# Performance work log

Hardware: AMD Instinct MI355X
Metric: run time of the kernel (lower is better)

## Reference

```python
import jax, jax.numpy as jnp
import numpy as np

SOM = (32, 32)   # som_dim; SOM[0]*SOM[1] == num_embeddings
LR = 0.05


def setup_inputs() -> dict:
    key = jax.random.key(0)
    k1, k2 = jax.random.split(key)
    B, K, D = 65536, 1024, 256
    x = jax.random.normal(k1, (B, D), dtype=jnp.float32)
    embeddings = jax.random.uniform(k2, (K, D), dtype=jnp.float32)  # torch.rand init
    return {"x": x, "embeddings": embeddings}


def reference(x, embeddings):
    K, D = embeddings.shape
    # pairwise squared distances: [B, K]
    dist = (jnp.sum(x * x, axis=1, keepdims=True)
            + jnp.sum(embeddings * embeddings, axis=1)
            - 2.0 * (x @ embeddings.T))
    n_min = jnp.argmin(dist, axis=1)          # [B]
    z_q = embeddings[n_min]                   # [B, D]

    # SOM grid coordinates and clamped neighbors
    n_x = n_min // SOM[1]
    n_y = n_min % SOM[1]
    x_up = jnp.where(n_x < SOM[0] - 1, n_x + 1, n_x)
    x_down = jnp.where(n_x > 0, n_x - 1, n_x)
    y_right = jnp.where(n_y < SOM[1] - 1, n_y + 1, n_y)
    y_left = jnp.where(n_y > 0, n_y - 1, n_y)
    idx_up = x_up * SOM[1] + n_y
    idx_down = x_down * SOM[1] + n_y
    idx_right = n_x * SOM[1] + y_right
    idx_left = n_x * SOM[1] + y_left

    # [B, 4, D] neighbor gather (order: up, down, left, right as in torch code)
    nbr_idx = jnp.stack([idx_up, idx_down, idx_left, idx_right], axis=1)
    z_q_neighbors = embeddings[nbr_idx]

    # SOM scatter update (torch does one-hot matmuls; segment_sum is the fused form)
    dw = x - z_q                              # [B, D]
    seg = lambda idx: jax.ops.segment_sum(dw, idx, num_segments=K)
    new_embeddings = jax.lax.stop_gradient(
        embeddings
        + LR * seg(n_min)
        + 0.5 * LR * (seg(idx_up) + seg(idx_down) + seg(idx_right) + seg(idx_left))
    )

    commit_loss = jnp.mean((x - z_q) ** 2)
    som_loss = jnp.mean((jax.lax.stop_gradient(x)[:, None, :] - z_q_neighbors) ** 2)
    return z_q, commit_loss, som_loss, new_embeddings
```

## Files before the change

### kernel.cpp

```cpp
#include <hip/hip_runtime.h>

#define B_ROWS 65536
#define DDIM   256
#define KEMB   1024
#define LRC    0.05f
#define BM 64
#define BN 128

typedef __attribute__((ext_vector_type(8))) _Float16 half8;
typedef __attribute__((ext_vector_type(4))) float f32x4;

#define SX_OFF    0u
#define CNT_OFF   1048576u
#define SUMS_OFF  1052672u
#define ESQ_OFF   1053312u
#define CUR_OFF   1057408u
#define NMIN_OFF  1061504u
#define ROWS_OFF  1585792u
#define EH_OFF    1847936u

static __device__ __forceinline__ unsigned short f2h(float f) {
  _Float16 h = (_Float16)f;
  return *(unsigned short*)&h;
}
static __device__ __forceinline__ float h2f(unsigned short u) {
  _Float16 h = *(_Float16*)&u;
  return (float)h;
}
static __device__ __forceinline__ void glds16(const void* g, void* l) {
  __builtin_amdgcn_global_load_lds(
      (const __attribute__((address_space(1))) unsigned int*)g,
      (__attribute__((address_space(3))) unsigned int*)l, 16, 0, 0);
}

__global__ __launch_bounds__(256) void convert_kernel(
    const float* __restrict__ E, unsigned short* __restrict__ Eh,
    float* __restrict__ esq) {
  size_t i = (size_t)blockIdx.x * 256 + threadIdx.x;
  size_t off = i * 8;
  const float4 v0 = *(const float4*)(E + off);
  const float4 v1 = *(const float4*)(E + off + 4);
  float f[8] = {v0.x, v0.y, v0.z, v0.w, v1.x, v1.y, v1.z, v1.w};
  unsigned short h[8];
  float part = 0.f;
#pragma unroll
  for (int j = 0; j < 8; ++j) {
    h[j] = f2h(f[j]);
    part += f[j] * f[j];
  }
  *(uint4*)(Eh + off) = *(const uint4*)h;
  float s = part;
  for (int o = 16; o > 0; o >>= 1) s += __shfl_down(s, o, 32);
  if ((threadIdx.x & 31) == 0) esq[i >> 5] = s;
}

__global__ __launch_bounds__(256, 2) void gemm_argmin_kernel(
    const float* __restrict__ X, const unsigned short* __restrict__ EhW,
    const float* __restrict__ esq, const float* __restrict__ Ef,
    int* __restrict__ nmin, int* __restrict__ counts, float* __restrict__ zq,
    double* __restrict__ sums, int bm_base) {
  __shared__ __align__(16) unsigned short sX[2][8][256][8];
  __shared__ __align__(16) unsigned short sE[2][512][8];

  const int tid  = threadIdx.x;
  const int lane = tid & 63, w = tid >> 6;
  const int lrow = lane & 15;
  const int qidx = lane >> 4;
  const int rowbase = (w >> 1) * 32;
  const int colb    = (w & 1) * 64;
  const int bm0 = (bm_base + (int)blockIdx.x) * BM;

  int ec_row[2], ec_q8[2];
#pragma unroll
  for (int j = 0; j < 2; ++j) {
    const int c = j * 256 + tid;
    ec_row[j] = c >> 2;
    ec_q8[j]  = ((c & 3) ^ ((ec_row[j] >> 1) & 3)) * 8;
  }

#pragma unroll
  for (int j = 0; j < 2; ++j)
    glds16(EhW + (size_t)ec_row[j] * DDIM + ec_q8[j], (char*)&sE[0][j * 256 + tid][0]);

  {
    float part = 0.f;
#pragma unroll
    for (int it = 0; it < 8; ++it) {
      const int c   = it * 256 + tid;
      const int kcc = c >> 8;
      const int cc  = c & 255;
      const int row = cc >> 2;
      const int q   = (cc & 3) ^ ((row >> 1) & 3);
      const float* xp = X + (size_t)(bm0 + row) * DDIM + kcc * 32 + q * 8;
      const float4 a = *(const float4*)xp;
      const float4 b = *(const float4*)(xp + 4);
      float f[8] = {a.x, a.y, a.z, a.w, b.x, b.y, b.z, b.w};
      unsigned short hh[8], ll[8];
#pragma unroll
      for (int m = 0; m < 8; ++m) {
        hh[m] = f2h(f[m]);
        ll[m] = f2h(f[m] - h2f(hh[m]));
        part += f[m] * f[m];
      }
      *(uint4*)((char*)sX + (size_t)c * 16)          = *(const uint4*)hh;
      *(uint4*)((char*)sX + (size_t)(c + 2048) * 16) = *(const uint4*)ll;
    }
#pragma unroll
    for (int o = 32; o > 0; o >>= 1) part += __shfl_down(part, o);
    if (lane == 0)
      atomicAdd(&sums[8 + (((int)blockIdx.x * 4 + w) & 63)], (double)part);
  }

  float rbest[8];
  int   ridx[8];
#pragma unroll
  for (int i = 0; i < 8; ++i) { rbest[i] = 3.4e38f; ridx[i] = 0; }

  int ra[2], rb[4];
#pragma unroll
  for (int t = 0; t < 2; ++t) {
    const int m = rowbase + t * 16 + lrow;
    ra[t] = (m << 2) | (qidx ^ ((m >> 1) & 3));
  }
#pragma unroll
  for (int t = 0; t < 4; ++t) {
    const int n = colb + t * 16 + lrow;
    rb[t] = (n << 2) | (qidx ^ ((n >> 1) & 3));
  }

  __syncthreads();

  for (int nt = 0; nt < 8; ++nt) {
    f32x4 acc[2][4];
#pragma unroll
    for (int i = 0; i < 2; ++i)
#pragma unroll
      for (int j = 0; j < 4; ++j) acc[i][j] = (f32x4){0.f, 0.f, 0.f, 0.f};

#pragma unroll
    for (int kcc = 0; kcc < 8; ++kcc) {
      const int s   = nt * 8 + kcc;
      const int cur = s & 1;
      if (s < 63) {
        const int ns = s + 1;
        const int nnt = ns >> 3, nk = ns & 7;
#pragma unroll
        for (int j = 0; j < 2; ++j) {
          const int c = j * 256 + tid;
          glds16(EhW + (size_t)(nnt * BN + ec_row[j]) * DDIM + nk * 32 + ec_q8[j],
                 (char*)&sE[cur ^ 1][c][0]);
        }
      }
      half8 af0[2], af1[2], bfr[4];
#pragma unroll
      for (int t = 0; t < 2; ++t) {
        af0[t] = *(const half8*)&sX[0][kcc][ra[t]][0];
        af1[t] = *(const half8*)&sX[1][kcc][ra[t]][0];
      }
#pragma unroll
      for (int t = 0; t < 4; ++t) bfr[t] = *(const half8*)&sE[cur][rb[t]][0];
#pragma unroll
      for (int tr = 0; tr < 2; ++tr)
#pragma unroll
        for (int tc = 0; tc < 4; ++tc)
          acc[tr][tc] = __builtin_amdgcn_mfma_f32_16x16x32_f16(
              af0[tr], bfr[tc], acc[tr][tc], 0, 0, 0);
#pragma unroll
      for (int tr = 0; tr < 2; ++tr)
#pragma unroll
        for (int tc = 0; tc < 4; ++tc)
          acc[tr][tc] = __builtin_amdgcn_mfma_f32_16x16x32_f16(
              af1[tr], bfr[tc], acc[tr][tc], 0, 0, 0);
      __syncthreads();
    }
#pragma unroll
    for (int tc = 0; tc < 4; ++tc) {
      const int col = nt * BN + colb + tc * 16 + lrow;
      const float eq = esq[col];
#pragma unroll
      for (int tr = 0; tr < 2; ++tr)
#pragma unroll
        for (int rr = 0; rr < 4; ++rr) {
          float d = eq - 2.0f * acc[tr][tc][rr];
          const int slot = tr * 4 + rr;
          if (d < rbest[slot]) { rbest[slot] = d; ridx[slot] = col; }
        }
    }
  }

  float* cdd = (float*)&sE[0][0][0];
  int*   cdi = (int*)(cdd + 128);
  int*   snm = cdi + 128;
  int*   h   = (int*)&sX[0][0][0][0];

#pragma unroll
  for (int i = 0; i < 4; ++i) h[tid + i * 256] = 0;

#pragma unroll
  for (int slot = 0; slot < 8; ++slot) {
    float bd = rbest[slot];
    int   bi = ridx[slot];
#pragma unroll
    for (int off = 1; off < 16; off <<= 1) {
      float od = __shfl_xor(bd, off, 64);
      int   oi = __shfl_xor(bi, off, 64);
      if (od < bd || (od == bd && oi < bi)) { bd = od; bi = oi; }
    }
    if (lrow == 0) {
      const int row = rowbase + (slot >> 2) * 16 + (lane >> 4) * 4 + (slot & 3);
      cdd[(w & 1) * 64 + row] = bd;
      cdi[(w & 1) * 64 + row] = bi;
    }
  }
  __syncthreads();
  if (tid < BM) {
    float d0 = cdd[tid], d1 = cdd[64 + tid];
    int   i0 = cdi[tid], i1 = cdi[64 + tid];
    int bi = (d1 < d0 || (d1 == d0 && i1 < i0)) ? i1 : i0;
    nmin[bm0 + tid] = bi;
    snm[tid] = bi;
    atomicAdd(&h[bi], 1);
  }
  __syncthreads();
#pragma unroll
  for (int i = 0; i < 4; ++i) {
    int v = h[tid + i * 256];
    if (v) atomicAdd(&counts[tid + i * 256], v);
  }
  const int r0 = w * 16;
#pragma unroll 4
  for (int r = 0; r < 16; ++r) {
    const int k = snm[r0 + r];
    const float4 v = *(const float4*)(Ef + (size_t)k * DDIM + lane * 4);
    *(float4*)(zq + (size_t)(bm0 + r0 + r) * DDIM + lane * 4) = v;
  }
}

__global__ __launch_bounds__(1024) void scatter_kernel(
    const int* __restrict__ counts, const int* __restrict__ nm,
    int* __restrict__ cur, int* __restrict__ rows) {
  __shared__ int lcnt[KEMB], lbase[KEMB], lrank[KEMB], scn[KEMB];
  int tid = threadIdx.x;
  lcnt[tid] = 0; lrank[tid] = 0;
  int v = counts[tid];
  scn[tid] = v;
  __syncthreads();
  for (int off = 1; off < 1024; off <<= 1) {
    int u = (tid >= off) ? scn[tid - off] : 0;
    __syncthreads();
    scn[tid] += u;
    __syncthreads();
  }
  int b = blockIdx.x * 1024 + tid;
  int k = nm[b];
  atomicAdd(&lcnt[k], 1);
  __syncthreads();
  if (lcnt[tid] > 0)
    lbase[tid] = (scn[tid] - v) + atomicAdd(&cur[tid], lcnt[tid]);
  __syncthreads();
  int r = atomicAdd(&lrank[k], 1);
  rows[lbase[k] + r] = b;
}

__global__ __launch_bounds__(256) void sxsum_kernel(
    const int* __restrict__ rows, const int* __restrict__ nm,
    const float* __restrict__ X, float* __restrict__ SX) {
  __shared__ int sb[32], sk[32];
  int tid = threadIdx.x;
  int p0 = blockIdx.x * 32;
  if (tid < 32) sb[tid] = rows[p0 + tid];
  __syncthreads();
  if (tid < 32) sk[tid] = nm[sb[tid]];
  __syncthreads();
  float acc = 0.f;
  int kprev = sk[0];
  for (int i = 0; i < 32; ++i) {
    int k = sk[i];
    if (k != kprev) {
      atomicAdd(&SX[(size_t)kprev * DDIM + tid], acc);
      acc = 0.f;
      kprev = k;
    }
    acc += X[(size_t)sb[i] * DDIM + tid];
  }
  atomicAdd(&SX[(size_t)kprev * DDIM + tid], acc);
}

__global__ __launch_bounds__(256) void stencil_kernel(
    const float* __restrict__ E, const float* __restrict__ SX,
    const int* __restrict__ counts, const float* __restrict__ esq,
    double* __restrict__ sums, float* __restrict__ out) {
  __shared__ float redc[256], reds[256];
  int k = blockIdx.x, t = threadIdx.x;
  int kx = k >> 5, ky = k & 31;
  int j1 = (kx >= 1)  ? k - 32 : k;
  int j2 = (kx <= 30) ? k + 32 : k;
  int j3 = (ky >= 1)  ? k - 1  : k;
  int j4 = (ky <= 30) ? k + 1  : k;
  int fU = (kx < 31) ? k + 32 : k;
  int fD = (kx > 0)  ? k - 32 : k;
  int fL = (ky > 0)  ? k - 1  : k;
  int fR = (ky < 31) ? k + 1  : k;

  float e   = E[(size_t)k * DDIM + t];
  float sxk = SX[(size_t)k * DDIM + t];
  float Tk = sxk - (float)counts[k] * e;
  float T1 = SX[(size_t)j1 * DDIM + t] - (float)counts[j1] * E[(size_t)j1 * DDIM + t];
  float T2 = SX[(size_t)j2 * DDIM + t] - (float)counts[j2] * E[(size_t)j2 * DDIM + t];
  float T3 = SX[(size_t)j3 * DDIM + t] - (float)counts[j3] * E[(size_t)j3 * DDIM + t];
  float T4 = SX[(size_t)j4 * DDIM + t] - (float)counts[j4] * E[(size_t)j4 * DDIM + t];
  float v = e + LRC * Tk + 0.5f * LRC * (T1 + T2 + T3 + T4);
  out[(size_t)B_ROWS * DDIM + 2 + (size_t)k * DDIM + t] = v;

  float eU = E[(size_t)fU * DDIM + t], eD = E[(size_t)fD * DDIM + t];
  float eL = E[(size_t)fL * DDIM + t], eR = E[(size_t)fR * DDIM + t];
  float cp = -2.f * sxk * e;
  float sp = -2.f * sxk * (eU + eD + eL + eR);
  if (t == 0) {
    float ck = (float)counts[k];
    cp += ck * esq[k];
    sp += ck * (esq[fU] + esq[fD] + esq[fL] + esq[fR]);
  }
  redc[t] = cp; reds[t] = sp;
  __syncthreads();
  for (int s = 128; s > 0; s >>= 1) {
    if (t < s) { redc[t] += redc[t + s]; reds[t] += reds[t + s]; }
    __syncthreads();
  }
  if (t == 0) {
    atomicAdd(&sums[1], (double)redc[0]);
    atomicAdd(&sums[2], (double)reds[0]);
    __threadfence();
    unsigned int prev = atomicAdd((unsigned int*)&sums[0], 1u);
    if (prev == KEMB - 1) {
      volatile const double* vs = (volatile const double*)sums;
      double xsq = 0.0;
#pragma unroll
      for (int s2 = 0; s2 < 64; ++s2) xsq += vs[8 + s2];
      double c1 = vs[1], c2 = vs[2];
      out[(size_t)B_ROWS * DDIM]     = (float)((xsq + c1) / ((double)B_ROWS * DDIM));
      out[(size_t)B_ROWS * DDIM + 1] =
          (float)((4.0 * xsq + c2) / ((double)B_ROWS * 4.0 * DDIM));
    }
  }
}

extern "C" void kernel_launch(void* const* d_in, const int* in_sizes, int n_in,
                              void* d_out, int out_size, void* d_ws, size_t ws_size,
                              hipStream_t stream) {
  const float* X = (const float*)d_in[0];
  const float* E = (const float*)d_in[1];
  float* out = (float*)d_out;
  char* ws = (char*)d_ws;

  float*          SX   = (float*)(ws + SX_OFF);
  int*            cnts = (int*)(ws + CNT_OFF);
  double*         sums = (double*)(ws + SUMS_OFF);
  float*          esq  = (float*)(ws + ESQ_OFF);
  int*            cur  = (int*)(ws + CUR_OFF);
  int*            nm   = (int*)(ws + NMIN_OFF);
  int*            rows = (int*)(ws + ROWS_OFF);
  unsigned short* EhW  = (unsigned short*)(ws + EH_OFF);

  hipMemsetAsync(ws, 0, NMIN_OFF, stream);

  convert_kernel<<<KEMB * (DDIM / 8) / 256, 256, 0, stream>>>(E, EhW, esq);
  gemm_argmin_kernel<<<512, 256, 0, stream>>>(X, EhW, esq, E, nm, cnts, out, sums, 0);
  gemm_argmin_kernel<<<512, 256, 0, stream>>>(X, EhW, esq, E, nm, cnts, out, sums, 512);
  scatter_kernel<<<B_ROWS / 1024, 1024, 0, stream>>>(cnts, nm, cur, rows);
  sxsum_kernel<<<B_ROWS / 32, 256, 0, stream>>>(rows, nm, X, SX);
  stencil_kernel<<<KEMB, 256, 0, stream>>>(E, SX, cnts, esq, sums, out);
}
```

Measured before the change: 274.3 us.

## Fuse per-code x sums into GEMM-argmin epilogue via atomics from LDS tile

Drops the separate counting-sort scatter and sorted-sum kernels. The GEMM-argmin epilogue now atomically adds each row's x into the per-code sum buffer, reading x back from the fp16 hi/lo split already held in shared memory. It also merges the two half-grid GEMM launches into one. This removes the nmin/rows round trips and two launches, but adds 256 float atomics per row to global memory, which can contend on popular codes. Rebuilding x from the fp16 hi+lo pair may also change precision slightly.

```diff
diff --git a/kernel.cpp b/kernel.cpp
--- a/kernel.cpp
+++ b/kernel.cpp
@@ -14,9 +14,6 @@
 #define CNT_OFF   1048576u
 #define SUMS_OFF  1052672u
 #define ESQ_OFF   1053312u
-#define CUR_OFF   1057408u
-#define NMIN_OFF  1061504u
-#define ROWS_OFF  1585792u
 #define EH_OFF    1847936u
 
 static __device__ __forceinline__ unsigned short f2h(float f) {
@@ -57,8 +54,8 @@
 __global__ __launch_bounds__(256, 2) void gemm_argmin_kernel(
     const float* __restrict__ X, const unsigned short* __restrict__ EhW,
     const float* __restrict__ esq, const float* __restrict__ Ef,
-    int* __restrict__ nmin, int* __restrict__ counts, float* __restrict__ zq,
-    double* __restrict__ sums, int bm_base) {
+    int* __restrict__ counts, float* __restrict__ zq,
+    double* __restrict__ sums, float* __restrict__ SX) {
   __shared__ __align__(16) unsigned short sX[2][8][256][8];
   __shared__ __align__(16) unsigned short sE[2][512][8];
 
@@ -68,7 +65,7 @@
   const int qidx = lane >> 4;
   const int rowbase = (w >> 1) * 32;
   const int colb    = (w & 1) * 64;
-  const int bm0 = (bm_base + (int)blockIdx.x) * BM;
+  const int bm0 = (int)blockIdx.x * BM;
 
   int ec_row[2], ec_q8[2];
 #pragma unroll
@@ -191,7 +188,7 @@
   float* cdd = (float*)&sE[0][0][0];
   int*   cdi = (int*)(cdd + 128);
   int*   snm = cdi + 128;
-  int*   h   = (int*)&sX[0][0][0][0];
+  int*   h   = snm + 64;
 
 #pragma unroll
   for (int i = 0; i < 4; ++i) h[tid + i * 256] = 0;
@@ -217,7 +214,6 @@
     float d0 = cdd[tid], d1 = cdd[64 + tid];
     int   i0 = cdi[tid], i1 = cdi[64 + tid];
     int bi = (d1 < d0 || (d1 == d0 && i1 < i0)) ? i1 : i0;
-    nmin[bm0 + tid] = bi;
     snm[tid] = bi;
     atomicAdd(&h[bi], 1);
   }
@@ -227,63 +223,26 @@
     int v = h[tid + i * 256];
     if (v) atomicAdd(&counts[tid + i * 256], v);
   }
+
   const int r0 = w * 16;
-#pragma unroll 4
+  const int kcc_r = lane >> 3;
+  const int q_r   = (lane >> 1) & 3;
+  const int e4_r  = (lane & 1) * 4;
+#pragma unroll 2
   for (int r = 0; r < 16; ++r) {
-    const int k = snm[r0 + r];
+    const int row = r0 + r;
+    const int k = snm[row];
+    const int ch = (row << 2) | (q_r ^ ((row >> 1) & 3));
+    const unsigned short* hp = &sX[0][kcc_r][ch][e4_r];
+    const unsigned short* lp = &sX[1][kcc_r][ch][e4_r];
+    float* dst = SX + (size_t)k * DDIM + lane * 4;
+    atomicAdd(dst + 0, h2f(hp[0]) + h2f(lp[0]));
+    atomicAdd(dst + 1, h2f(hp[1]) + h2f(lp[1]));
+    atomicAdd(dst + 2, h2f(hp[2]) + h2f(lp[2]));
+    atomicAdd(dst + 3, h2f(hp[3]) + h2f(lp[3]));
     const float4 v = *(const float4*)(Ef + (size_t)k * DDIM + lane * 4);
-    *(float4*)(zq + (size_t)(bm0 + r0 + r) * DDIM + lane * 4) = v;
-  }
-}
-
-__global__ __launch_bounds__(1024) void scatter_kernel(
-    const int* __restrict__ counts, const int* __restrict__ nm,
-    int* __restrict__ cur, int* __restrict__ rows) {
-  __shared__ int lcnt[KEMB], lbase[KEMB], lrank[KEMB], scn[KEMB];
-  int tid = threadIdx.x;
-  lcnt[tid] = 0; lrank[tid] = 0;
-  int v = counts[tid];
-  scn[tid] = v;
-  __syncthreads();
-  for (int off = 1; off < 1024; off <<= 1) {
-    int u = (tid >= off) ? scn[tid - off] : 0;
-    __syncthreads();
-    scn[tid] += u;
-    __syncthreads();
-  }
-  int b = blockIdx.x * 1024 + tid;
-  int k = nm[b];
-  atomicAdd(&lcnt[k], 1);
-  __syncthreads();
-  if (lcnt[tid] > 0)
-    lbase[tid] = (scn[tid] - v) + atomicAdd(&cur[tid], lcnt[tid]);
-  __syncthreads();
-  int r = atomicAdd(&lrank[k], 1);
-  rows[lbase[k] + r] = b;
-}
-
-__global__ __launch_bounds__(256) void sxsum_kernel(
-    const int* __restrict__ rows, const int* __restrict__ nm,
-    const float* __restrict__ X, float* __restrict__ SX) {
-  __shared__ int sb[32], sk[32];
-  int tid = threadIdx.x;
-  int p0 = blockIdx.x * 32;
-  if (tid < 32) sb[tid] = rows[p0 + tid];
-  __syncthreads();
-  if (tid < 32) sk[tid] = nm[sb[tid]];
-  __syncthreads();
-  float acc = 0.f;
-  int kprev = sk[0];
-  for (int i = 0; i < 32; ++i) {
-    int k = sk[i];
-    if (k != kprev) {
-      atomicAdd(&SX[(size_t)kprev * DDIM + tid], acc);
-      acc = 0.f;
-      kprev = k;
-    }
-    acc += X[(size_t)sb[i] * DDIM + tid];
-  }
-  atomicAdd(&SX[(size_t)kprev * DDIM + tid], acc);
+    *(float4*)(zq + (size_t)(bm0 + row) * DDIM + lane * 4) = v;
+  }
 }
 
 __global__ __launch_bounds__(256) void stencil_kernel(
@@ -357,17 +316,12 @@
   int*            cnts = (int*)(ws + CNT_OFF);
   double*         sums = (double*)(ws + SUMS_OFF);
   float*          esq  = (float*)(ws + ESQ_OFF);
-  int*            cur  = (int*)(ws + CUR_OFF);
-  int*            nm   = (int*)(ws + NMIN_OFF);
-  int*            rows = (int*)(ws + ROWS_OFF);
   unsigned short* EhW  = (unsigned short*)(ws + EH_OFF);
 
-  hipMemsetAsync(ws, 0, NMIN_OFF, stream);
+  hipMemsetAsync(ws, 0, ESQ_OFF, stream);
 
   convert_kernel<<<KEMB * (DDIM / 8) / 256, 256, 0, stream>>>(E, EhW, esq);
-  gemm_argmin_kernel<<<512, 256, 0, stream>>>(X, EhW, esq, E, nm, cnts, out, sums, 0);
-  gemm_argmin_kernel<<<512, 256, 0, stream>>>(X, EhW, esq, E, nm, cnts, out, sums, 512);
-  scatter_kernel<<<B_ROWS / 1024, 1024, 0, stream>>>(cnts, nm, cur, rows);
-  sxsum_kernel<<<B_ROWS / 32, 256, 0, stream>>>(rows, nm, X, SX);
+  gemm_argmin_kernel<<<B_ROWS / BM, 256, 0, stream>>>(X, EhW, esq, E, cnts, out,
+                                                      sums, SX);
   stencil_kernel<<<KEMB, 256, 0, stream>>>(E, SX, cnts, esq, sums, out);
 }
```

Measured after the change: 562.7 us. 2.05x slower.
